# Kernel tuning notes

Hardware: AMD Instinct MI355X
Metric: run time of the kernel (lower is better)

The kernel has to match this reference:

```python
import jax, jax.numpy as jnp
import numpy as np
import math

D_MODEL, N_HEADS, D_FF = 512, 8, 2048
B, S = 2, 2048
EPS = 1e-6


def _layernorm(x, g, b):
    mu = jnp.mean(x, axis=-1, keepdims=True)
    var = jnp.mean((x - mu) ** 2, axis=-1, keepdims=True)
    return (x - mu) * jax.lax.rsqrt(var + EPS) * g + b


def setup_inputs() -> dict:
    key = jax.random.key(0)
    ks = jax.random.split(key, 16)
    sd = 1.0 / math.sqrt(D_MODEL)
    return {
        "x": jax.random.normal(ks[0], (B, S, D_MODEL), jnp.float32),
        "sensor_weights": jax.random.uniform(ks[1], (B, S, 4), jnp.float32),
        "mask": jnp.ones((1, 1, S, S), jnp.int32),
        "Wq": jax.random.normal(ks[2], (D_MODEL, D_MODEL), jnp.float32) * sd,
        "Wk": jax.random.normal(ks[3], (D_MODEL, D_MODEL), jnp.float32) * sd,
        "Wv": jax.random.normal(ks[4], (D_MODEL, D_MODEL), jnp.float32) * sd,
        "Wo": jax.random.normal(ks[5], (D_MODEL, D_MODEL), jnp.float32) * sd,
        "bo": jnp.zeros((D_MODEL,), jnp.float32),
        "sensor_attention": jnp.ones((N_HEADS, 4), jnp.float32),  # init = ones
        "temporal_bias": jax.random.normal(ks[6], (1, N_HEADS, 1, 1), jnp.float32) * 0.02,
        "ln1_g": jnp.ones((D_MODEL,), jnp.float32),
        "ln1_b": jnp.zeros((D_MODEL,), jnp.float32),
        "ln2_g": jnp.ones((D_MODEL,), jnp.float32),
        "ln2_b": jnp.zeros((D_MODEL,), jnp.float32),
        "W1": jax.random.normal(ks[7], (D_MODEL, D_FF), jnp.float32) * sd,
        "b1": jnp.zeros((D_FF,), jnp.float32),
        "W2": jax.random.normal(ks[8], (D_FF, D_MODEL), jnp.float32) * (1.0 / math.sqrt(D_FF)),
        "b2": jnp.zeros((D_MODEL,), jnp.float32),
    }


def reference(x, sensor_weights, mask, Wq, Wk, Wv, Wo, bo, sensor_attention,
              temporal_bias, ln1_g, ln1_b, ln2_g, ln2_b, W1, b1, W2, b2):
    b, s, d = x.shape
    h = temporal_bias.shape[1]
    dk = d // h
    scale = math.sqrt(dk)

    # [b, h, s, dk]
    q = (x @ Wq).reshape(b, s, h, dk).transpose(0, 2, 1, 3)
    k = (x @ Wk).reshape(b, s, h, dk).transpose(0, 2, 1, 3)
    v = (x @ Wv).reshape(b, s, h, dk).transpose(0, 2, 1, 3)

    scores = jnp.einsum('bhqd,bhkd->bhqk', q, k) / scale  # [b,h,s,s]
    scores = scores + temporal_bias
    # sensor bias: [h,4] x [b,s,4] -> [b,h,s], added per query row
    sensor_bias = jnp.einsum('hf,bsf->bhs', sensor_attention, sensor_weights)
    scores = scores + sensor_bias[..., None]
    scores = jnp.where(mask == 0, jnp.asarray(-1e9, scores.dtype), scores)

    attn = jax.nn.softmax(scores, axis=-1)
    ctx = jnp.einsum('bhqk,bhkd->bhqd', attn, v)
    ctx = ctx.transpose(0, 2, 1, 3).reshape(b, s, d)
    attn_out = ctx @ Wo + bo

    x1 = _layernorm(x + attn_out, ln1_g, ln1_b)
    ff = jax.nn.gelu(x1 @ W1 + b1, approximate=False) @ W2 + b2
    x2 = _layernorm(x1 + ff, ln2_g, ln2_b)
    return x2, attn
```

## Files before the change

kernel.cpp:

```cpp
#include <hip/hip_runtime.h>
#include <cstdint>
#include <cstddef>

#define S_LEN 2048
#define DM 512
#define NH 8
#define DK 64
#define DFF 2048
#define BATCH 2
#define NROWS (BATCH*S_LEN)
#define BHN (BATCH*NH)

#define MASKED_L2 (-1.4426950408889634e9f)
#define QSCALE 0.18033688011112042f

typedef __attribute__((ext_vector_type(8))) _Float16 f16x8;
typedef __attribute__((ext_vector_type(4))) float f32x4;

#define MFMA(a,b,c) __builtin_amdgcn_mfma_f32_16x16x32_f16(a,b,c,0,0,0)

__device__ __forceinline__ unsigned short f2h(float x){
  union{ _Float16 h; unsigned short u; } c; c.h = (_Float16)x; return c.u;
}
__device__ __forceinline__ int sw64(int r, int c){
  return r*64 + ((((c>>3) ^ r) & 7)<<3) + (c&7);
}
__device__ __forceinline__ int sw32(int r, int c){
  return r*32 + ((((c>>3) ^ r) & 3)<<3) + (c&7);
}

__global__ __launch_bounds__(256) void prep_kernel(
    const float* __restrict__ x, const int* __restrict__ mask,
    const float* __restrict__ Wq, const float* __restrict__ Wk,
    const float* __restrict__ Wv, const float* __restrict__ Wo,
    const float* __restrict__ W1, const float* __restrict__ W2,
    unsigned short* __restrict__ xb,
    unsigned short* __restrict__ wqT, unsigned short* __restrict__ wkT,
    unsigned short* __restrict__ wvT, unsigned short* __restrict__ woT,
    unsigned short* __restrict__ w1T, unsigned short* __restrict__ w2T,
    unsigned* __restrict__ maskw)
{
  const int z = blockIdx.y;
  const int t = blockIdx.x;
  const int tid = threadIdx.x;
  if (z < 6){
    const float* W; unsigned short* WT; int K, N;
    switch(z){
      case 0: W=Wq; WT=wqT; K=512;  N=512;  break;
      case 1: W=Wk; WT=wkT; K=512;  N=512;  break;
      case 2: W=Wv; WT=wvT; K=512;  N=512;  break;
      case 3: W=Wo; WT=woT; K=512;  N=512;  break;
      case 4: W=W1; WT=w1T; K=512;  N=2048; break;
      default:W=W2; WT=w2T; K=2048; N=512;  break;
    }
    const int ntiles = N>>5, ktiles = K>>5;
    if (t >= ntiles*ktiles) return;
    const int kt = t / ntiles, nt = t - kt*ntiles;
    __shared__ float tile[32][33];
    const int tx = tid & 31, ty = tid >> 5;
    #pragma unroll
    for (int i=0;i<4;i++){
      int r = ty + i*8;
      tile[r][tx] = W[(size_t)(kt*32 + r)*N + nt*32 + tx];
    }
    __syncthreads();
    #pragma unroll
    for (int i=0;i<4;i++){
      int r = ty + i*8;
      WT[(size_t)(nt*32 + r)*K + kt*32 + tx] = f2h(tile[tx][r]);
    }
  } else if (z == 6){
    size_t base = (size_t)t*2048 + (size_t)tid*8;
    float4 a = *(const float4*)(x + base);
    float4 b = *(const float4*)(x + base + 4);
    union{ unsigned short h[8]; uint4 v; } pk;
    pk.h[0]=f2h(a.x); pk.h[1]=f2h(a.y); pk.h[2]=f2h(a.z); pk.h[3]=f2h(a.w);
    pk.h[4]=f2h(b.x); pk.h[5]=f2h(b.y); pk.h[6]=f2h(b.z); pk.h[7]=f2h(b.w);
    *(uint4*)(xb + base) = pk.v;
  } else {
    if (t >= 512) return;
    const int gid = t*256 + tid;
    const int row = gid >> 6, w = gid & 63;
    const int4* mp = (const int4*)(mask + (size_t)row*2048 + w*32);
    unsigned word = 0;
    #pragma unroll
    for (int j=0;j<8;j++){
      int4 v = mp[j];
      word |= (unsigned)(v.x!=0) << (j*4+0);
      word |= (unsigned)(v.y!=0) << (j*4+1);
      word |= (unsigned)(v.z!=0) << (j*4+2);
      word |= (unsigned)(v.w!=0) << (j*4+3);
    }
    maskw[gid] = word;
  }
}

template<int KD, int EPI>
__global__ __launch_bounds__(256) void gemm_kernel(
    const unsigned short* __restrict__ A,
    const unsigned short* __restrict__ BT0,
    const unsigned short* __restrict__ BT1,
    const unsigned short* __restrict__ BT2,
    const float* __restrict__ bias,
    const float* __restrict__ resid,
    float* __restrict__ outf,
    unsigned short* __restrict__ ob0,
    unsigned short* __restrict__ ob1,
    unsigned short* __restrict__ ob2)
{
  const unsigned short* BT = BT0;
  unsigned short* outb = ob0;
  float scale = 1.0f;
  if (EPI == 0){
    const int z = blockIdx.z;
    if (z == 0) scale = QSCALE;
    else if (z == 1){ BT = BT1; outb = ob1; }
    else            { BT = BT2; outb = ob2; }
  }
  const int m0 = blockIdx.x*64, n0 = blockIdx.y*64;
  const int tid = threadIdx.x;
  const int wid = tid>>6, l = tid&63, quad = l>>4, lc = l&15;
  const int wm = wid&1, wn = wid>>1;
  __shared__ __align__(16) unsigned short As[2][64*32];
  __shared__ __align__(16) unsigned short Bs[2][64*32];
  const int sr = tid>>2, sc = (tid&3)*8;
  const unsigned short* Ap = A  + (size_t)(m0+sr)*KD + sc;
  const unsigned short* Bp = BT + (size_t)(n0+sr)*KD + sc;
  {
    uint4 va = *(const uint4*)Ap;
    uint4 vb = *(const uint4*)Bp;
    *(uint4*)&As[0][sw32(sr,sc)] = va;
    *(uint4*)&Bs[0][sw32(sr,sc)] = vb;
  }
  f32x4 acc00={0,0,0,0}, acc01={0,0,0,0}, acc10={0,0,0,0}, acc11={0,0,0,0};
  const int ar0 = wm*32 + lc, ar1 = wm*32 + 16 + lc;
  const int br0 = wn*32 + lc, br1 = wn*32 + 16 + lc;
  __syncthreads();
  constexpr int NK = KD/32;
  for (int kk=0; kk<NK; kk++){
    const int cur = kk & 1;
    if (kk+1 < NK){
      uint4 va = *(const uint4*)(Ap + (size_t)(kk+1)*32);
      uint4 vb = *(const uint4*)(Bp + (size_t)(kk+1)*32);
      *(uint4*)&As[cur^1][sw32(sr,sc)] = va;
      *(uint4*)&Bs[cur^1][sw32(sr,sc)] = vb;
    }
    f16x8 a0 = *(const f16x8*)&As[cur][sw32(ar0, quad*8)];
    f16x8 a1 = *(const f16x8*)&As[cur][sw32(ar1, quad*8)];
    f16x8 b0 = *(const f16x8*)&Bs[cur][sw32(br0, quad*8)];
    f16x8 b1 = *(const f16x8*)&Bs[cur][sw32(br1, quad*8)];
    acc00 = MFMA(a0,b0,acc00);
    acc01 = MFMA(a0,b1,acc01);
    acc10 = MFMA(a1,b0,acc10);
    acc11 = MFMA(a1,b1,acc11);
    __syncthreads();
  }
  f32x4 accs[2][2] = {{acc00,acc01},{acc10,acc11}};
  #pragma unroll
  for (int mt=0;mt<2;mt++){
    #pragma unroll
    for (int nt=0;nt<2;nt++){
      f32x4 v = accs[mt][nt];
      const int col  = n0 + wn*32 + nt*16 + lc;
      const int row0 = m0 + wm*32 + mt*16 + quad*4;
      #pragma unroll
      for (int r=0;r<4;r++){
        const int row = row0 + r;
        const float val = v[r];
        if (EPI == 0){
          const int h = col>>6, d = col&63, b = row>>11, s = row&2047;
          outb[(((size_t)(b*NH + h))*S_LEN + s)*DK + d] = f2h(val*scale);
        } else if (EPI == 1){
          const size_t idx = (size_t)row*DM + col;
          outf[idx] = val + bias[col] + resid[idx];
        } else {
          const float xx = val + bias[col];
          const float gg = 0.5f*xx*(1.0f + erff(xx*0.70710678118654752f));
          outb[(size_t)row*DFF + col] = f2h(gg);
        }
      }
    }
  }
}

__global__ __launch_bounds__(256) void kml_kernel(
    const unsigned short* __restrict__ qw,
    const unsigned short* __restrict__ kw,
    const unsigned* __restrict__ maskw,
    float* __restrict__ m_out, float* __restrict__ li_out)
{
  const int bh = blockIdx.y, q0 = blockIdx.x*64;
  const int tid = threadIdx.x, wid = tid>>6, l = tid&63, quad = l>>4, lc = l&15;
  __shared__ __align__(16) unsigned short Qs[64*64];
  __shared__ __align__(16) unsigned short Ks[2][64*64];
  const unsigned short* qbase = qw + ((size_t)bh*S_LEN + q0)*DK;
  const unsigned short* kbase = kw + (size_t)bh*S_LEN*DK;
  #pragma unroll
  for (int i=0;i<2;i++){
    const int idx = tid + i*256, r = idx>>3, c0 = (idx&7)*8;
    *(uint4*)&Qs[sw64(r,c0)]    = *(const uint4*)(qbase + (size_t)r*DK + c0);
    *(uint4*)&Ks[0][sw64(r,c0)] = *(const uint4*)(kbase + (size_t)r*DK + c0);
  }
  __syncthreads();
  f16x8 aQ0, aQ1;
  {
    const int r = wid*16 + lc;
    aQ0 = *(const f16x8*)&Qs[sw64(r, quad*8)];
    aQ1 = *(const f16x8*)&Qs[sw64(r, 32 + quad*8)];
  }
  float m[4]  = {-3e38f,-3e38f,-3e38f,-3e38f};
  float ls[4] = {0.f,0.f,0.f,0.f};
  const int rowb = q0 + wid*16 + quad*4;
  for (int c=0;c<32;c++){
    const int cur = c & 1;
    if (c+1 < 32){
      #pragma unroll
      for (int i=0;i<2;i++){
        const int idx = tid + i*256, r = idx>>3, c0 = (idx&7)*8;
        *(uint4*)&Ks[cur^1][sw64(r,c0)] =
          *(const uint4*)(kbase + ((size_t)(c+1)*64 + r)*DK + c0);
      }
    }
    uint2 mw[4];
    #pragma unroll
    for (int r=0;r<4;r++)
      mw[r] = *(const uint2*)(maskw + (size_t)(rowb+r)*64 + c*2);
    float sv[4][4];
    #pragma unroll
    for (int nt=0; nt<4; nt++){
      f16x8 b0 = *(const f16x8*)&Ks[cur][sw64(nt*16+lc, quad*8)];
      f16x8 b1 = *(const f16x8*)&Ks[cur][sw64(nt*16+lc, 32+quad*8)];
      f32x4 s = {0,0,0,0};
      s = MFMA(aQ0, b0, s);
      s = MFMA(aQ1, b1, s);
      const int sh = (nt&1)*16 + lc;
      #pragma unroll
      for (int r=0;r<4;r++){
        const unsigned w = (nt<2) ? mw[r].x : mw[r].y;
        sv[nt][r] = ((w>>sh)&1u) ? s[r] : MASKED_L2;
      }
    }
    #pragma unroll
    for (int r=0;r<4;r++){
      const float mc = fmaxf(fmaxf(sv[0][r],sv[1][r]), fmaxf(sv[2][r],sv[3][r]));
      const float m2 = fmaxf(m[r], mc);
      ls[r] = ls[r]*__builtin_exp2f(m[r]-m2)
            + __builtin_exp2f(sv[0][r]-m2) + __builtin_exp2f(sv[1][r]-m2)
            + __builtin_exp2f(sv[2][r]-m2) + __builtin_exp2f(sv[3][r]-m2);
      m[r] = m2;
    }
    __syncthreads();
  }
  #pragma unroll
  for (int o=1;o<16;o<<=1){
    #pragma unroll
    for (int r=0;r<4;r++){
      const float mo = __shfl_xor(m[r], o, 64);
      const float lo = __shfl_xor(ls[r], o, 64);
      const float m2 = fmaxf(m[r], mo);
      ls[r] = ls[r]*__builtin_exp2f(m[r]-m2) + lo*__builtin_exp2f(mo-m2);
      m[r] = m2;
    }
  }
  if (lc == 0){
    const size_t rowg = (size_t)bh*S_LEN + rowb;
    #pragma unroll
    for (int r=0;r<4;r++){
      m_out[rowg+r]  = m[r];
      li_out[rowg+r] = 1.0f/ls[r];
    }
  }
}

__global__ __launch_bounds__(256) void kattn_kernel(
    const unsigned short* __restrict__ qw,
    const unsigned short* __restrict__ kw,
    const unsigned short* __restrict__ vw,
    const unsigned* __restrict__ maskw,
    const float* __restrict__ m_in,
    const float* __restrict__ li_in,
    float* __restrict__ attn,
    unsigned short* __restrict__ ctx)
{
  const int bh = blockIdx.y, q0 = blockIdx.x*64;
  const int tid = threadIdx.x, wid = tid>>6, l = tid&63, quad = l>>4, lc = l&15;
  __shared__ __align__(16) unsigned short Qs[64*64];
  __shared__ __align__(16) unsigned short Ks[2][64*64];
  __shared__ __align__(16) unsigned short Vs[2][64*64];
  __shared__ __align__(16) unsigned short Ps[4][16*64];
  const unsigned short* qbase = qw + ((size_t)bh*S_LEN + q0)*DK;
  const unsigned short* kbase = kw + (size_t)bh*S_LEN*DK;
  const unsigned short* vbase = vw + (size_t)bh*S_LEN*DK;
  #pragma unroll
  for (int i=0;i<2;i++){
    const int idx = tid + i*256, r = idx>>3, c0 = (idx&7)*8;
    *(uint4*)&Qs[sw64(r,c0)]    = *(const uint4*)(qbase + (size_t)r*DK + c0);
    *(uint4*)&Ks[0][sw64(r,c0)] = *(const uint4*)(kbase + (size_t)r*DK + c0);
    union { uint4 u; unsigned short h[8]; } U;
    U.u = *(const uint4*)(vbase + (size_t)r*DK + c0);
    #pragma unroll
    for (int j=0;j<8;j++) Vs[0][sw64(c0+j, r)] = U.h[j];
  }
  __syncthreads();
  f16x8 aQ0, aQ1;
  {
    const int r = wid*16 + lc;
    aQ0 = *(const f16x8*)&Qs[sw64(r, quad*8)];
    aQ1 = *(const f16x8*)&Qs[sw64(r, 32 + quad*8)];
  }
  const int rowb = q0 + wid*16 + quad*4;
  float mr[4], li[4];
  #pragma unroll
  for (int r=0;r<4;r++){
    mr[r] = m_in[(size_t)bh*S_LEN + rowb + r];
    li[r] = li_in[(size_t)bh*S_LEN + rowb + r];
  }
  f32x4 O0={0,0,0,0}, O1={0,0,0,0}, O2={0,0,0,0}, O3={0,0,0,0};
  float* attnbase = attn + (size_t)bh*S_LEN*S_LEN;
  unsigned short* myP = &Ps[wid][0];
  for (int c=0;c<32;c++){
    const int cur = c & 1;
    if (c+1 < 32){
      #pragma unroll
      for (int i=0;i<2;i++){
        const int idx = tid + i*256, r = idx>>3, c0 = (idx&7)*8;
        *(uint4*)&Ks[cur^1][sw64(r,c0)] =
          *(const uint4*)(kbase + ((size_t)(c+1)*64 + r)*DK + c0);
        union { uint4 u; unsigned short h[8]; } U;
        U.u = *(const uint4*)(vbase + ((size_t)(c+1)*64 + r)*DK + c0);
        #pragma unroll
        for (int j=0;j<8;j++) Vs[cur^1][sw64(c0+j, r)] = U.h[j];
      }
    }
    uint2 mw[4];
    #pragma unroll
    for (int r=0;r<4;r++)
      mw[r] = *(const uint2*)(maskw + (size_t)(rowb+r)*64 + c*2);
    #pragma unroll
    for (int nt=0; nt<4; nt++){
      f16x8 b0 = *(const f16x8*)&Ks[cur][sw64(nt*16+lc, quad*8)];
      f16x8 b1 = *(const f16x8*)&Ks[cur][sw64(nt*16+lc, 32+quad*8)];
      f32x4 s = {0,0,0,0};
      s = MFMA(aQ0, b0, s);
      s = MFMA(aQ1, b1, s);
      const int sh = (nt&1)*16 + lc;
      #pragma unroll
      for (int r=0;r<4;r++){
        const unsigned w = (nt<2) ? mw[r].x : mw[r].y;
        const float se = ((w>>sh)&1u) ? s[r] : MASKED_L2;
        const float p  = __builtin_exp2f(se - mr[r]) * li[r];
        __builtin_nontemporal_store(p,
          attnbase + (size_t)(rowb+r)*S_LEN + (size_t)c*64 + nt*16 + lc);
        myP[sw64(quad*4+r, nt*16+lc)] = f2h(p);
      }
    }
    #pragma unroll
    for (int ks=0; ks<2; ks++){
      f16x8 aP = *(const f16x8*)&myP[sw64(lc, ks*32 + quad*8)];
      f16x8 v0 = *(const f16x8*)&Vs[cur][sw64( 0+lc, ks*32+quad*8)];
      f16x8 v1 = *(const f16x8*)&Vs[cur][sw64(16+lc, ks*32+quad*8)];
      f16x8 v2 = *(const f16x8*)&Vs[cur][sw64(32+lc, ks*32+quad*8)];
      f16x8 v3 = *(const f16x8*)&Vs[cur][sw64(48+lc, ks*32+quad*8)];
      O0 = MFMA(aP, v0, O0);
      O1 = MFMA(aP, v1, O1);
      O2 = MFMA(aP, v2, O2);
      O3 = MFMA(aP, v3, O3);
    }
    __syncthreads();
  }
  const int b = bh>>3, h = bh&7;
  f32x4 Os[4] = {O0,O1,O2,O3};
  #pragma unroll
  for (int nt=0; nt<4; nt++){
    #pragma unroll
    for (int r=0;r<4;r++){
      ctx[((size_t)b*S_LEN + rowb + r)*DM + h*DK + nt*16 + lc] = f2h(Os[nt][r]);
    }
  }
}

__global__ __launch_bounds__(256) void ln_kernel(
    const float* __restrict__ in, const float* __restrict__ g,
    const float* __restrict__ b, float* __restrict__ outf,
    unsigned short* __restrict__ outb)
{
  const int row = blockIdx.x*4 + (threadIdx.x>>6);
  const int l = threadIdx.x & 63;
  const float* p = in + (size_t)row*DM + l*8;
  float4 v0 = *(const float4*)p;
  float4 v1 = *(const float4*)(p+4);
  float vals[8] = {v0.x,v0.y,v0.z,v0.w,v1.x,v1.y,v1.z,v1.w};
  float s = 0.f, q = 0.f;
  #pragma unroll
  for (int j=0;j<8;j++){ s += vals[j]; q += vals[j]*vals[j]; }
  #pragma unroll
  for (int o=1;o<64;o<<=1){ s += __shfl_xor(s,o,64); q += __shfl_xor(q,o,64); }
  const float mu = s*(1.0f/DM);
  const float var = q*(1.0f/DM) - mu*mu;
  const float rs = rsqrtf(var + 1e-6f);
  const float* gp = g + l*8;
  const float* bp = b + l*8;
  float4 g0 = *(const float4*)gp, g1 = *(const float4*)(gp+4);
  float4 bb0 = *(const float4*)bp, bb1 = *(const float4*)(bp+4);
  float gv[8] = {g0.x,g0.y,g0.z,g0.w,g1.x,g1.y,g1.z,g1.w};
  float bv[8] = {bb0.x,bb0.y,bb0.z,bb0.w,bb1.x,bb1.y,bb1.z,bb1.w};
  float ov[8];
  #pragma unroll
  for (int j=0;j<8;j++) ov[j] = (vals[j]-mu)*rs*gv[j] + bv[j];
  float* op = outf + (size_t)row*DM + l*8;
  *(float4*)op     = make_float4(ov[0],ov[1],ov[2],ov[3]);
  *(float4*)(op+4) = make_float4(ov[4],ov[5],ov[6],ov[7]);
  if (outb){
    union{ unsigned short h[8]; uint4 v; } pk;
    #pragma unroll
    for (int j=0;j<8;j++) pk.h[j] = f2h(ov[j]);
    *(uint4*)(outb + (size_t)row*DM + l*8) = pk.v;
  }
}

extern "C" void kernel_launch(void* const* d_in, const int* in_sizes, int n_in,
                              void* d_out, int out_size, void* d_ws, size_t ws_size,
                              hipStream_t stream)
{
  const float* x    = (const float*)d_in[0];
  const int*   mask = (const int*)d_in[2];
  const float* Wq   = (const float*)d_in[3];
  const float* Wk   = (const float*)d_in[4];
  const float* Wv   = (const float*)d_in[5];
  const float* Wo   = (const float*)d_in[6];
  const float* bo   = (const float*)d_in[7];
  const float* ln1g = (const float*)d_in[10];
  const float* ln1b = (const float*)d_in[11];
  const float* ln2g = (const float*)d_in[12];
  const float* ln2b = (const float*)d_in[13];
  const float* W1   = (const float*)d_in[14];
  const float* b1   = (const float*)d_in[15];
  const float* W2   = (const float*)d_in[16];
  const float* b2   = (const float*)d_in[17];

  float* x2_out   = (float*)d_out;
  float* attn_out = x2_out + (size_t)NROWS*DM;

  char* p = (char*)d_ws;
  auto alloc = [&](size_t bytes)->char*{
    char* r = p; p += (bytes + 255) & ~(size_t)255; return r;
  };
  unsigned short* xb   = (unsigned short*)alloc((size_t)NROWS*DM*2);
  unsigned short* wqT  = (unsigned short*)alloc(512*512*2);
  unsigned short* wkT  = (unsigned short*)alloc(512*512*2);
  unsigned short* wvT  = (unsigned short*)alloc(512*512*2);
  unsigned short* woT  = (unsigned short*)alloc(512*512*2);
  unsigned short* w1T  = (unsigned short*)alloc(2048*512*2);
  unsigned short* w2T  = (unsigned short*)alloc(512*2048*2);
  unsigned short* q_ws = (unsigned short*)alloc((size_t)BHN*S_LEN*DK*2);
  unsigned short* k_ws = (unsigned short*)alloc((size_t)BHN*S_LEN*DK*2);
  unsigned short* v_ws = (unsigned short*)alloc((size_t)BHN*S_LEN*DK*2);
  unsigned*       maskw= (unsigned*)alloc((size_t)S_LEN*64*4);
  float*          m_ws = (float*)alloc((size_t)BHN*S_LEN*4);
  float*          li_ws= (float*)alloc((size_t)BHN*S_LEN*4);
  unsigned short* ctxb = (unsigned short*)alloc((size_t)NROWS*DM*2);
  float*          yv   = (float*)alloc((size_t)NROWS*DM*4);
  float*          x1f  = (float*)alloc((size_t)NROWS*DM*4);
  unsigned short* x1b  = (unsigned short*)alloc((size_t)NROWS*DM*2);
  unsigned short* hb   = (unsigned short*)alloc((size_t)NROWS*DFF*2);
  float*          zv   = (float*)alloc((size_t)NROWS*DM*4);

  prep_kernel<<<dim3(1024,8), 256, 0, stream>>>(
      x, mask, Wq, Wk, Wv, Wo, W1, W2,
      xb, wqT, wkT, wvT, woT, w1T, w2T, maskw);

  gemm_kernel<512,0><<<dim3(64,8,3), 256, 0, stream>>>(
      xb, wqT, wkT, wvT, nullptr, nullptr, nullptr, q_ws, k_ws, v_ws);

  kml_kernel<<<dim3(32,16), 256, 0, stream>>>(q_ws, k_ws, maskw, m_ws, li_ws);

  kattn_kernel<<<dim3(32,16), 256, 0, stream>>>(
      q_ws, k_ws, v_ws, maskw, m_ws, li_ws, attn_out, ctxb);

  gemm_kernel<512,1><<<dim3(64,8), 256, 0, stream>>>(
      ctxb, woT, nullptr, nullptr, bo, x, yv, nullptr, nullptr, nullptr);

  ln_kernel<<<1024, 256, 0, stream>>>(yv, ln1g, ln1b, x1f, x1b);

  gemm_kernel<512,2><<<dim3(64,32), 256, 0, stream>>>(
      x1b, w1T, nullptr, nullptr, b1, nullptr, nullptr, hb, nullptr, nullptr);

  gemm_kernel<2048,1><<<dim3(64,8), 256, 0, stream>>>(
      hb, w2T, nullptr, nullptr, b2, x1f, zv, nullptr, nullptr, nullptr);

  ln_kernel<<<1024, 256, 0, stream>>>(zv, ln2g, ln2b, x2_out, nullptr);

  (void)in_sizes; (void)n_in; (void)out_size; (void)ws_size;
}
```

Before: 543.9 us.

## Fuse softmax stats pass into attention kernel and use transposed S^T formulation

Merges the separate row-max/sum kernel into the attention kernel as a first pass, removing a launch and the m/li workspace round-trip. The score MFMA is flipped to compute K·Q^T so each lane owns one query row, which makes per-row statistics lane-local and allows float4 nontemporal stores of the attention matrix. The QKV GEMM now writes V transposed, so P feeds a 16x16x16 MFMA straight from registers instead of going through a shared-memory P buffer. s_setprio hints are added around the MFMA regions. The trade-off is more MFMA instructions, since the smaller-K MFMA replaces the 32-wide one.

```diff
diff --git a/kernel.cpp b/kernel.cpp
--- a/kernel.cpp
+++ b/kernel.cpp
@@ -15,9 +15,11 @@
 #define QSCALE 0.18033688011112042f
 
 typedef __attribute__((ext_vector_type(8))) _Float16 f16x8;
+typedef __attribute__((ext_vector_type(4))) _Float16 f16x4;
 typedef __attribute__((ext_vector_type(4))) float f32x4;
 
-#define MFMA(a,b,c) __builtin_amdgcn_mfma_f32_16x16x32_f16(a,b,c,0,0,0)
+#define MFMA(a,b,c)   __builtin_amdgcn_mfma_f32_16x16x32_f16(a,b,c,0,0,0)
+#define MFMA16(a,b,c) __builtin_amdgcn_mfma_f32_16x16x16f16(a,b,c,0,0,0)
 
 __device__ __forceinline__ unsigned short f2h(float x){
   union{ _Float16 h; unsigned short u; } c; c.h = (_Float16)x; return c.u;
@@ -111,11 +113,12 @@
   const unsigned short* BT = BT0;
   unsigned short* outb = ob0;
   float scale = 1.0f;
+  bool vtrans = false;
   if (EPI == 0){
     const int z = blockIdx.z;
     if (z == 0) scale = QSCALE;
     else if (z == 1){ BT = BT1; outb = ob1; }
-    else            { BT = BT2; outb = ob2; }
+    else            { BT = BT2; outb = ob2; vtrans = true; }
   }
   const int m0 = blockIdx.x*64, n0 = blockIdx.y*64;
   const int tid = threadIdx.x;
@@ -163,111 +166,30 @@
       f32x4 v = accs[mt][nt];
       const int col  = n0 + wn*32 + nt*16 + lc;
       const int row0 = m0 + wm*32 + mt*16 + quad*4;
-      #pragma unroll
-      for (int r=0;r<4;r++){
-        const int row = row0 + r;
-        const float val = v[r];
-        if (EPI == 0){
-          const int h = col>>6, d = col&63, b = row>>11, s = row&2047;
-          outb[(((size_t)(b*NH + h))*S_LEN + s)*DK + d] = f2h(val*scale);
-        } else if (EPI == 1){
-          const size_t idx = (size_t)row*DM + col;
-          outf[idx] = val + bias[col] + resid[idx];
-        } else {
-          const float xx = val + bias[col];
-          const float gg = 0.5f*xx*(1.0f + erff(xx*0.70710678118654752f));
-          outb[(size_t)row*DFF + col] = f2h(gg);
+      if (EPI == 0 && vtrans){
+        const int h = col>>6, d = col&63, b = row0>>11, s0 = row0&2047;
+        union{ unsigned short h4[4]; uint2 u; } pk;
+        #pragma unroll
+        for (int r=0;r<4;r++) pk.h4[r] = f2h(v[r]);
+        *(uint2*)(outb + (((size_t)(b*NH + h))*DK + d)*S_LEN + s0) = pk.u;
+      } else {
+        #pragma unroll
+        for (int r=0;r<4;r++){
+          const int row = row0 + r;
+          const float val = v[r];
+          if (EPI == 0){
+            const int h = col>>6, d = col&63, b = row>>11, s = row&2047;
+            outb[(((size_t)(b*NH + h))*S_LEN + s)*DK + d] = f2h(val*scale);
+          } else if (EPI == 1){
+            const size_t idx = (size_t)row*DM + col;
+            outf[idx] = val + bias[col] + resid[idx];
+          } else {
+            const float xx = val + bias[col];
+            const float gg = 0.5f*xx*(1.0f + erff(xx*0.70710678118654752f));
+            outb[(size_t)row*DFF + col] = f2h(gg);
+          }
         }
       }
-    }
-  }
-}
-
-__global__ __launch_bounds__(256) void kml_kernel(
-    const unsigned short* __restrict__ qw,
-    const unsigned short* __restrict__ kw,
-    const unsigned* __restrict__ maskw,
-    float* __restrict__ m_out, float* __restrict__ li_out)
-{
-  const int bh = blockIdx.y, q0 = blockIdx.x*64;
-  const int tid = threadIdx.x, wid = tid>>6, l = tid&63, quad = l>>4, lc = l&15;
-  __shared__ __align__(16) unsigned short Qs[64*64];
-  __shared__ __align__(16) unsigned short Ks[2][64*64];
-  const unsigned short* qbase = qw + ((size_t)bh*S_LEN + q0)*DK;
-  const unsigned short* kbase = kw + (size_t)bh*S_LEN*DK;
-  #pragma unroll
-  for (int i=0;i<2;i++){
-    const int idx = tid + i*256, r = idx>>3, c0 = (idx&7)*8;
-    *(uint4*)&Qs[sw64(r,c0)]    = *(const uint4*)(qbase + (size_t)r*DK + c0);
-    *(uint4*)&Ks[0][sw64(r,c0)] = *(const uint4*)(kbase + (size_t)r*DK + c0);
-  }
-  __syncthreads();
-  f16x8 aQ0, aQ1;
-  {
-    const int r = wid*16 + lc;
-    aQ0 = *(const f16x8*)&Qs[sw64(r, quad*8)];
-    aQ1 = *(const f16x8*)&Qs[sw64(r, 32 + quad*8)];
-  }
-  float m[4]  = {-3e38f,-3e38f,-3e38f,-3e38f};
-  float ls[4] = {0.f,0.f,0.f,0.f};
-  const int rowb = q0 + wid*16 + quad*4;
-  for (int c=0;c<32;c++){
-    const int cur = c & 1;
-    if (c+1 < 32){
-      #pragma unroll
-      for (int i=0;i<2;i++){
-        const int idx = tid + i*256, r = idx>>3, c0 = (idx&7)*8;
-        *(uint4*)&Ks[cur^1][sw64(r,c0)] =
-          *(const uint4*)(kbase + ((size_t)(c+1)*64 + r)*DK + c0);
-      }
-    }
-    uint2 mw[4];
-    #pragma unroll
-    for (int r=0;r<4;r++)
-      mw[r] = *(const uint2*)(maskw + (size_t)(rowb+r)*64 + c*2);
-    float sv[4][4];
-    #pragma unroll
-    for (int nt=0; nt<4; nt++){
-      f16x8 b0 = *(const f16x8*)&Ks[cur][sw64(nt*16+lc, quad*8)];
-      f16x8 b1 = *(const f16x8*)&Ks[cur][sw64(nt*16+lc, 32+quad*8)];
-      f32x4 s = {0,0,0,0};
-      s = MFMA(aQ0, b0, s);
-      s = MFMA(aQ1, b1, s);
-      const int sh = (nt&1)*16 + lc;
-      #pragma unroll
-      for (int r=0;r<4;r++){
-        const unsigned w = (nt<2) ? mw[r].x : mw[r].y;
-        sv[nt][r] = ((w>>sh)&1u) ? s[r] : MASKED_L2;
-      }
-    }
-    #pragma unroll
-    for (int r=0;r<4;r++){
-      const float mc = fmaxf(fmaxf(sv[0][r],sv[1][r]), fmaxf(sv[2][r],sv[3][r]));
-      const float m2 = fmaxf(m[r], mc);
-      ls[r] = ls[r]*__builtin_exp2f(m[r]-m2)
-            + __builtin_exp2f(sv[0][r]-m2) + __builtin_exp2f(sv[1][r]-m2)
-            + __builtin_exp2f(sv[2][r]-m2) + __builtin_exp2f(sv[3][r]-m2);
-      m[r] = m2;
-    }
-    __syncthreads();
-  }
-  #pragma unroll
-  for (int o=1;o<16;o<<=1){
-    #pragma unroll
-    for (int r=0;r<4;r++){
-      const float mo = __shfl_xor(m[r], o, 64);
-      const float lo = __shfl_xor(ls[r], o, 64);
-      const float m2 = fmaxf(m[r], mo);
-      ls[r] = ls[r]*__builtin_exp2f(m[r]-m2) + lo*__builtin_exp2f(mo-m2);
-      m[r] = m2;
-    }
-  }
-  if (lc == 0){
-    const size_t rowg = (size_t)bh*S_LEN + rowb;
-    #pragma unroll
-    for (int r=0;r<4;r++){
-      m_out[rowg+r]  = m[r];
-      li_out[rowg+r] = 1.0f/ls[r];
     }
   }
 }
@@ -275,10 +197,8 @@
 __global__ __launch_bounds__(256) void kattn_kernel(
     const unsigned short* __restrict__ qw,
     const unsigned short* __restrict__ kw,
-    const unsigned short* __restrict__ vw,
+    const unsigned short* __restrict__ vwT,
     const unsigned* __restrict__ maskw,
-    const float* __restrict__ m_in,
-    const float* __restrict__ li_in,
     float* __restrict__ attn,
     unsigned short* __restrict__ ctx)
 {
@@ -287,95 +207,143 @@
   __shared__ __align__(16) unsigned short Qs[64*64];
   __shared__ __align__(16) unsigned short Ks[2][64*64];
   __shared__ __align__(16) unsigned short Vs[2][64*64];
-  __shared__ __align__(16) unsigned short Ps[4][16*64];
   const unsigned short* qbase = qw + ((size_t)bh*S_LEN + q0)*DK;
   const unsigned short* kbase = kw + (size_t)bh*S_LEN*DK;
-  const unsigned short* vbase = vw + (size_t)bh*S_LEN*DK;
+  const unsigned short* vbase = vwT + (size_t)bh*DK*S_LEN;
+
+  auto stageK = [&](unsigned short* dst, const unsigned short* src){
+    #pragma unroll
+    for (int i=0;i<2;i++){
+      const int idx = tid + i*256, r = idx>>3, c0 = (idx&7)*8;
+      *(uint4*)&dst[sw64(r,c0)] = *(const uint4*)(src + (size_t)r*DK + c0);
+    }
+  };
+  auto stageV = [&](unsigned short* dst, const unsigned short* src){
+    #pragma unroll
+    for (int i=0;i<2;i++){
+      const int idx = tid + i*256, d = idx>>3, k0 = (idx&7)*8;
+      union { uint4 u; uint2 v2[2]; } U;
+      U.u = *(const uint4*)(src + (size_t)d*S_LEN + k0);
+      const int g0 = k0>>2;
+      *(uint2*)&dst[(g0  )*256 + (((d ^  g0   )&63)<<2)] = U.v2[0];
+      *(uint2*)&dst[(g0+1)*256 + (((d ^ (g0+1))&63)<<2)] = U.v2[1];
+    }
+  };
+
   #pragma unroll
   for (int i=0;i<2;i++){
     const int idx = tid + i*256, r = idx>>3, c0 = (idx&7)*8;
-    *(uint4*)&Qs[sw64(r,c0)]    = *(const uint4*)(qbase + (size_t)r*DK + c0);
-    *(uint4*)&Ks[0][sw64(r,c0)] = *(const uint4*)(kbase + (size_t)r*DK + c0);
-    union { uint4 u; unsigned short h[8]; } U;
-    U.u = *(const uint4*)(vbase + (size_t)r*DK + c0);
-    #pragma unroll
-    for (int j=0;j<8;j++) Vs[0][sw64(c0+j, r)] = U.h[j];
-  }
+    *(uint4*)&Qs[sw64(r,c0)] = *(const uint4*)(qbase + (size_t)r*DK + c0);
+  }
+  stageK(Ks[0], kbase);
   __syncthreads();
-  f16x8 aQ0, aQ1;
+
+  f16x8 bQ0, bQ1;
   {
     const int r = wid*16 + lc;
-    aQ0 = *(const f16x8*)&Qs[sw64(r, quad*8)];
-    aQ1 = *(const f16x8*)&Qs[sw64(r, 32 + quad*8)];
-  }
-  const int rowb = q0 + wid*16 + quad*4;
-  float mr[4], li[4];
-  #pragma unroll
-  for (int r=0;r<4;r++){
-    mr[r] = m_in[(size_t)bh*S_LEN + rowb + r];
-    li[r] = li_in[(size_t)bh*S_LEN + rowb + r];
-  }
-  f32x4 O0={0,0,0,0}, O1={0,0,0,0}, O2={0,0,0,0}, O3={0,0,0,0};
-  float* attnbase = attn + (size_t)bh*S_LEN*S_LEN;
-  unsigned short* myP = &Ps[wid][0];
+    bQ0 = *(const f16x8*)&Qs[sw64(r, quad*8)];
+    bQ1 = *(const f16x8*)&Qs[sw64(r, 32 + quad*8)];
+  }
+  const int rowq = q0 + wid*16 + lc;
+  const unsigned* mrow = maskw + (size_t)rowq*64;
+
+  float m = -3e38f, ls = 0.f;
+  for (int c=0;c<32;c++){
+    const int cur = c & 1;
+    if (c+1 < 32) stageK(Ks[cur^1], kbase + (size_t)(c+1)*64*DK);
+    const uint2 mw = *(const uint2*)(mrow + c*2);
+    float sv[4][4];
+    __builtin_amdgcn_s_setprio(1);
+    #pragma unroll
+    for (int nt=0; nt<4; nt++){
+      f16x8 aK0 = *(const f16x8*)&Ks[cur][sw64(nt*16+lc, quad*8)];
+      f16x8 aK1 = *(const f16x8*)&Ks[cur][sw64(nt*16+lc, 32+quad*8)];
+      f32x4 s = {0,0,0,0};
+      s = MFMA(aK0, bQ0, s);
+      s = MFMA(aK1, bQ1, s);
+      const unsigned w = (nt<2) ? mw.x : mw.y;
+      #pragma unroll
+      for (int r=0;r<4;r++){
+        const int sh = (nt&1)*16 + quad*4 + r;
+        sv[nt][r] = ((w>>sh)&1u) ? s[r] : MASKED_L2;
+      }
+    }
+    __builtin_amdgcn_s_setprio(0);
+    float mc = sv[0][0];
+    #pragma unroll
+    for (int nt=0;nt<4;nt++)
+      #pragma unroll
+      for (int r=0;r<4;r++) mc = fmaxf(mc, sv[nt][r]);
+    const float m2 = fmaxf(m, mc);
+    float add = 0.f;
+    #pragma unroll
+    for (int nt=0;nt<4;nt++)
+      #pragma unroll
+      for (int r=0;r<4;r++) add += __builtin_exp2f(sv[nt][r]-m2);
+    ls = ls*__builtin_exp2f(m-m2) + add;
+    m = m2;
+    __syncthreads();
+  }
+  #pragma unroll
+  for (int o=16;o<64;o<<=1){
+    const float mo = __shfl_xor(m, o, 64);
+    const float lo = __shfl_xor(ls, o, 64);
+    const float m2 = fmaxf(m, mo);
+    ls = ls*__builtin_exp2f(m-m2) + lo*__builtin_exp2f(mo-m2);
+    m = m2;
+  }
+  const float li = 1.0f/ls;
+
+  stageK(Ks[0], kbase);
+  stageV(Vs[0], vbase);
+  f32x4 O[4] = {{0,0,0,0},{0,0,0,0},{0,0,0,0},{0,0,0,0}};
+  float* arow = attn + (size_t)bh*S_LEN*S_LEN + (size_t)rowq*S_LEN;
+  __syncthreads();
   for (int c=0;c<32;c++){
     const int cur = c & 1;
     if (c+1 < 32){
-      #pragma unroll
-      for (int i=0;i<2;i++){
-        const int idx = tid + i*256, r = idx>>3, c0 = (idx&7)*8;
-        *(uint4*)&Ks[cur^1][sw64(r,c0)] =
-          *(const uint4*)(kbase + ((size_t)(c+1)*64 + r)*DK + c0);
-        union { uint4 u; unsigned short h[8]; } U;
-        U.u = *(const uint4*)(vbase + ((size_t)(c+1)*64 + r)*DK + c0);
-        #pragma unroll
-        for (int j=0;j<8;j++) Vs[cur^1][sw64(c0+j, r)] = U.h[j];
-      }
-    }
-    uint2 mw[4];
-    #pragma unroll
-    for (int r=0;r<4;r++)
-      mw[r] = *(const uint2*)(maskw + (size_t)(rowb+r)*64 + c*2);
+      stageK(Ks[cur^1], kbase + (size_t)(c+1)*64*DK);
+      stageV(Vs[cur^1], vbase + (size_t)(c+1)*64);
+    }
+    const uint2 mw = *(const uint2*)(mrow + c*2);
+    __builtin_amdgcn_s_setprio(1);
     #pragma unroll
     for (int nt=0; nt<4; nt++){
-      f16x8 b0 = *(const f16x8*)&Ks[cur][sw64(nt*16+lc, quad*8)];
-      f16x8 b1 = *(const f16x8*)&Ks[cur][sw64(nt*16+lc, 32+quad*8)];
+      f16x8 aK0 = *(const f16x8*)&Ks[cur][sw64(nt*16+lc, quad*8)];
+      f16x8 aK1 = *(const f16x8*)&Ks[cur][sw64(nt*16+lc, 32+quad*8)];
       f32x4 s = {0,0,0,0};
-      s = MFMA(aQ0, b0, s);
-      s = MFMA(aQ1, b1, s);
-      const int sh = (nt&1)*16 + lc;
+      s = MFMA(aK0, bQ0, s);
+      s = MFMA(aK1, bQ1, s);
+      const unsigned w = (nt<2) ? mw.x : mw.y;
+      f32x4 pv;
+      f16x4 bP;
       #pragma unroll
       for (int r=0;r<4;r++){
-        const unsigned w = (nt<2) ? mw[r].x : mw[r].y;
+        const int sh = (nt&1)*16 + quad*4 + r;
         const float se = ((w>>sh)&1u) ? s[r] : MASKED_L2;
-        const float p  = __builtin_exp2f(se - mr[r]) * li[r];
-        __builtin_nontemporal_store(p,
-          attnbase + (size_t)(rowb+r)*S_LEN + (size_t)c*64 + nt*16 + lc);
-        myP[sw64(quad*4+r, nt*16+lc)] = f2h(p);
+        const float p  = __builtin_exp2f(se - m) * li;
+        pv[r] = p;
+        bP[r] = (_Float16)p;
       }
-    }
-    #pragma unroll
-    for (int ks=0; ks<2; ks++){
-      f16x8 aP = *(const f16x8*)&myP[sw64(lc, ks*32 + quad*8)];
-      f16x8 v0 = *(const f16x8*)&Vs[cur][sw64( 0+lc, ks*32+quad*8)];
-      f16x8 v1 = *(const f16x8*)&Vs[cur][sw64(16+lc, ks*32+quad*8)];
-      f16x8 v2 = *(const f16x8*)&Vs[cur][sw64(32+lc, ks*32+quad*8)];
-      f16x8 v3 = *(const f16x8*)&Vs[cur][sw64(48+lc, ks*32+quad*8)];
-      O0 = MFMA(aP, v0, O0);
-      O1 = MFMA(aP, v1, O1);
-      O2 = MFMA(aP, v2, O2);
-      O3 = MFMA(aP, v3, O3);
-    }
+      __builtin_nontemporal_store(pv, (f32x4*)(arow + (size_t)c*64 + nt*16 + quad*4));
+      const int g = nt*4 + quad;
+      #pragma unroll
+      for (int dt=0; dt<4; dt++){
+        f16x4 aV = *(const f16x4*)&Vs[cur][g*256 + ((((dt*16+lc) ^ g)&63)<<2)];
+        O[dt] = MFMA16(aV, bP, O[dt]);
+      }
+    }
+    __builtin_amdgcn_s_setprio(0);
     __syncthreads();
   }
   const int b = bh>>3, h = bh&7;
-  f32x4 Os[4] = {O0,O1,O2,O3};
-  #pragma unroll
-  for (int nt=0; nt<4; nt++){
-    #pragma unroll
-    for (int r=0;r<4;r++){
-      ctx[((size_t)b*S_LEN + rowb + r)*DM + h*DK + nt*16 + lc] = f2h(Os[nt][r]);
-    }
+  unsigned short* cb = ctx + ((size_t)b*S_LEN + rowq)*DM + h*DK + quad*4;
+  #pragma unroll
+  for (int dt=0; dt<4; dt++){
+    union{ unsigned short h4[4]; uint2 u; } pk;
+    #pragma unroll
+    for (int r=0;r<4;r++) pk.h4[r] = f2h(O[dt][r]);
+    *(uint2*)(cb + dt*16) = pk.u;
   }
 }
 
@@ -456,8 +424,6 @@
   unsigned short* k_ws = (unsigned short*)alloc((size_t)BHN*S_LEN*DK*2);
   unsigned short* v_ws = (unsigned short*)alloc((size_t)BHN*S_LEN*DK*2);
   unsigned*       maskw= (unsigned*)alloc((size_t)S_LEN*64*4);
-  float*          m_ws = (float*)alloc((size_t)BHN*S_LEN*4);
-  float*          li_ws= (float*)alloc((size_t)BHN*S_LEN*4);
   unsigned short* ctxb = (unsigned short*)alloc((size_t)NROWS*DM*2);
   float*          yv   = (float*)alloc((size_t)NROWS*DM*4);
   float*          x1f  = (float*)alloc((size_t)NROWS*DM*4);
@@ -472,10 +438,8 @@
   gemm_kernel<512,0><<<dim3(64,8,3), 256, 0, stream>>>(
       xb, wqT, wkT, wvT, nullptr, nullptr, nullptr, q_ws, k_ws, v_ws);
 
-  kml_kernel<<<dim3(32,16), 256, 0, stream>>>(q_ws, k_ws, maskw, m_ws, li_ws);
-
   kattn_kernel<<<dim3(32,16), 256, 0, stream>>>(
-      q_ws, k_ws, v_ws, maskw, m_ws, li_ws, attn_out, ctxb);
+      q_ws, k_ws, v_ws, maskw, attn_out, ctxb);
 
   gemm_kernel<512,1><<<dim3(64,8), 256, 0, stream>>>(
       ctxb, woT, nullptr, nullptr, bo, x, yv, nullptr, nullptr, nullptr);
```

After: 497.9 us. 8.5% less time.
